# Kernel tuning notes

Hardware: AMD Instinct MI355X
Metric: run time of the kernel (lower is better)

Reference implementation:

```python
import jax, jax.numpy as jnp
import numpy as np

DIM = 96
HEADS = 6
HEAD_DIM = DIM // HEADS
WIN = 8
N = WIN * WIN           # tokens per window
B_ = 4096               # num_windows * batch
TABLE = (2 * WIN - 1) ** 2  # 225


def setup_inputs() -> dict:
    key = jax.random.key(0)
    ks = jax.random.split(key, 7)
    x = jax.random.normal(ks[0], (B_, N, DIM), dtype=jnp.float32)
    rpi = jax.random.randint(ks[1], (N, N), 0, TABLE)
    qkv_w = jax.random.normal(ks[2], (3 * DIM, DIM), dtype=jnp.float32) * 0.02
    qkv_b = jnp.zeros((3 * DIM,), dtype=jnp.float32)
    proj_w = jax.random.normal(ks[3], (DIM, DIM), dtype=jnp.float32) * 0.02
    proj_b = jnp.zeros((DIM,), dtype=jnp.float32)
    rpb_table = jax.random.normal(ks[4], (TABLE, HEADS), dtype=jnp.float32) * 0.02
    return {"x": x, "rpi": rpi, "qkv_w": qkv_w, "qkv_b": qkv_b,
            "proj_w": proj_w, "proj_b": proj_b, "rpb_table": rpb_table}


def reference(x, rpi, qkv_w, qkv_b, proj_w, proj_b, rpb_table):
    b_, n, c = x.shape
    scale = HEAD_DIM ** -0.5
    # qkv projection: (b_, n, 3, H, hd)
    qkv = (x @ qkv_w.T + qkv_b).reshape(b_, n, 3, HEADS, HEAD_DIM)
    qkv = jnp.transpose(qkv, (2, 0, 3, 1, 4))  # (3, b_, H, n, hd)
    q, k, v = qkv[0], qkv[1], qkv[2]
    attn = jnp.einsum('bhnd,bhmd->bhnm', q * scale, k)
    # relative position bias gather: (n, n, H) -> (H, n, n)
    bias = jnp.transpose(rpb_table[rpi], (2, 0, 1))
    attn = jax.nn.softmax(attn + bias[None], axis=-1)
    out = jnp.einsum('bhnm,bhmd->bnhd', attn, v).reshape(b_, n, c)
    return out @ proj_w.T + proj_b
```

## Files before the change

kernel.cpp:

```cpp
#include <hip/hip_runtime.h>

#define NWIN 4096
#define DIM 96
#define HEADS 6
#define NTOK 64

typedef __bf16 bf16x8 __attribute__((ext_vector_type(8)));
typedef __bf16 bf16x4 __attribute__((ext_vector_type(4)));
typedef short  s16x4  __attribute__((ext_vector_type(4)));
typedef float  f32x4  __attribute__((ext_vector_type(4)));

#define WS_QKVW 0
#define WS_PROJW 55296
#define WS_BIAS 73728
#define WS_TOTAL 172032

__device__ __forceinline__ f32x4 mfma32(bf16x8 a, bf16x8 b, f32x4 c) {
  return __builtin_amdgcn_mfma_f32_16x16x32_bf16(a, b, c, 0, 0, 0);
}
__device__ __forceinline__ f32x4 mfma16k(bf16x4 a, bf16x4 b, f32x4 c) {
  return __builtin_amdgcn_mfma_f32_16x16x16bf16_1k(
      __builtin_bit_cast(s16x4, a), __builtin_bit_cast(s16x4, b), c, 0, 0, 0);
}

__device__ __forceinline__ bf16x8 cvt8(const float* p) {
  const float4* q = (const float4*)p;
  float4 a = q[0];
  float4 b = q[1];
  bf16x8 r;
  r[0] = (__bf16)a.x; r[1] = (__bf16)a.y; r[2] = (__bf16)a.z; r[3] = (__bf16)a.w;
  r[4] = (__bf16)b.x; r[5] = (__bf16)b.y; r[6] = (__bf16)b.z; r[7] = (__bf16)b.w;
  return r;
}

__global__ void prep_kernel(const float* __restrict__ qkv_w,
                            const float* __restrict__ proj_w,
                            const float* __restrict__ rpb,
                            const int* __restrict__ rpi,
                            char* __restrict__ ws) {
  int i = blockIdx.x * blockDim.x + threadIdx.x;
  __bf16* qw = (__bf16*)(ws + WS_QKVW);
  __bf16* pw = (__bf16*)(ws + WS_PROJW);
  float* bias = (float*)(ws + WS_BIAS);
  if (i < 288 * 96) qw[i] = (__bf16)qkv_w[i];
  int j = i - 288 * 96;
  if (j >= 0 && j < 96 * 96) pw[j] = (__bf16)proj_w[j];
  int t = i - (288 * 96 + 96 * 96);
  if (t >= 0 && t < HEADS * 16 * 64 * 4) {
    int r = t & 3;
    int lane = (t >> 2) & 63;
    int ba = (t >> 8) & 15;
    int h = t >> 12;
    int bq = ba >> 2, a = ba & 3;
    int l16 = lane & 15, lq = lane >> 4;
    int qrow = 16 * bq + l16;
    int kcol = 16 * a + 4 * lq + r;
    bias[t] = rpb[rpi[qrow * 64 + kcol] * HEADS + h];
  }
}

template <bool USE_WS>
__global__ __launch_bounds__(128, 4) void win_attn(
    const float* __restrict__ x,
    const int* __restrict__ rpi,
    const float* __restrict__ qkv_w,
    const float* __restrict__ qkv_b,
    const float* __restrict__ proj_w,
    const float* __restrict__ proj_b,
    const float* __restrict__ rpb,
    const char* __restrict__ ws,
    float* __restrict__ out) {
  __shared__ __align__(16) __bf16 xfrag[6144];
  __shared__ __align__(16) __bf16 ao[64 * 104];

  const int tid = (int)threadIdx.x;
  const int wv = tid >> 6;
  const int lane = tid & 63;
  const int l16 = lane & 15;
  const int lq = lane >> 4;
  const int b = (int)blockIdx.x;

  const float* xw = x + (size_t)b * (NTOK * DIM);
  const __bf16* qwb = (const __bf16*)(ws + WS_QKVW);
  const __bf16* pwb = (const __bf16*)(ws + WS_PROJW);

#pragma unroll
  for (int ff = 0; ff < 6; ++ff) {
    const int mt = 2 * wv + ff / 3;
    const int ks = ff % 3;
    const int f = 6 * wv + ff;
    bf16x8 v = cvt8(xw + (16 * mt + l16) * DIM + 32 * ks + 8 * lq);
    *(bf16x8*)(xfrag + (f * 64 + lane) * 8) = v;
  }
  __syncthreads();

#define XV(mt, ks) (*(const bf16x8*)(xfrag + (((mt) * 3 + (ks)) * 64 + lane) * 8))

#pragma unroll 1
  for (int hh = 0; hh < 3; ++hh) {
    const int h = wv + 2 * hh;

    bf16x4 kb[4];
    {
      const int frow = (HEADS + h) * 16;
      bf16x8 wb[3];
#pragma unroll
      for (int ks = 0; ks < 3; ++ks) {
        if constexpr (USE_WS)
          wb[ks] = *(const bf16x8*)(qwb + (frow + l16) * 96 + 32 * ks + 8 * lq);
        else
          wb[ks] = cvt8(qkv_w + (frow + l16) * 96 + 32 * ks + 8 * lq);
      }
      const float4 kb4 = *(const float4*)(qkv_b + frow + 4 * lq);
      const float kbv[4] = {kb4.x, kb4.y, kb4.z, kb4.w};
#pragma unroll
      for (int mt = 0; mt < 4; ++mt) {
        f32x4 acc = {0.f, 0.f, 0.f, 0.f};
#pragma unroll
        for (int ks = 0; ks < 3; ++ks) acc = mfma32(wb[ks], XV(mt, ks), acc);
#pragma unroll
        for (int r = 0; r < 4; ++r) kb[mt][r] = (__bf16)(acc[r] + kbv[r]);
      }
    }

    bf16x4 qv4[4];
    {
      const int frow = h * 16;
      bf16x8 wb[3];
#pragma unroll
      for (int ks = 0; ks < 3; ++ks) {
        if constexpr (USE_WS)
          wb[ks] = *(const bf16x8*)(qwb + (frow + l16) * 96 + 32 * ks + 8 * lq);
        else
          wb[ks] = cvt8(qkv_w + (frow + l16) * 96 + 32 * ks + 8 * lq);
      }
      const float4 qb4 = *(const float4*)(qkv_b + frow + 4 * lq);
      const float qbv[4] = {qb4.x, qb4.y, qb4.z, qb4.w};
#pragma unroll
      for (int mt = 0; mt < 4; ++mt) {
        f32x4 acc = {0.f, 0.f, 0.f, 0.f};
#pragma unroll
        for (int ks = 0; ks < 3; ++ks) acc = mfma32(wb[ks], XV(mt, ks), acc);
#pragma unroll
        for (int r = 0; r < 4; ++r)
          qv4[mt][r] = (__bf16)((acc[r] + qbv[r]) * 0.25f);
      }
    }

    bf16x4 vb4[4];
    {
      const int frow = (2 * HEADS + h) * 16;
      bf16x8 wb[3];
#pragma unroll
      for (int ks = 0; ks < 3; ++ks) {
        if constexpr (USE_WS)
          wb[ks] = *(const bf16x8*)(qwb + (frow + l16) * 96 + 32 * ks + 8 * lq);
        else
          wb[ks] = cvt8(qkv_w + (frow + l16) * 96 + 32 * ks + 8 * lq);
      }
      const float vb = qkv_b[frow + l16];
#pragma unroll
      for (int mt = 0; mt < 4; ++mt) {
        f32x4 acc = {0.f, 0.f, 0.f, 0.f};
#pragma unroll
        for (int ks = 0; ks < 3; ++ks) acc = mfma32(XV(mt, ks), wb[ks], acc);
#pragma unroll
        for (int r = 0; r < 4; ++r) vb4[mt][r] = (__bf16)(acc[r] + vb);
      }
    }

    const float4* bias4 = (const float4*)(ws + WS_BIAS) + (h << 10);
#pragma unroll
    for (int bq = 0; bq < 4; ++bq) {
      f32x4 s[4];
      if constexpr (USE_WS) {
#pragma unroll
        for (int a = 0; a < 4; ++a) {
          float4 t = bias4[(bq * 4 + a) * 64 + lane];
          s[a][0] = t.x; s[a][1] = t.y; s[a][2] = t.z; s[a][3] = t.w;
        }
      } else {
#pragma unroll
        for (int a = 0; a < 4; ++a)
#pragma unroll
          for (int r = 0; r < 4; ++r)
            s[a][r] = rpb[rpi[(16 * bq + l16) * 64 + 16 * a + 4 * lq + r] *
                              HEADS + h];
      }

#pragma unroll
      for (int a = 0; a < 4; ++a) s[a] = mfma16k(kb[a], qv4[bq], s[a]);

      float tp[4];
      bf16x4 pa[4];
#pragma unroll
      for (int a = 0; a < 4; ++a) {
        float t0 = 0.f;
#pragma unroll
        for (int r = 0; r < 4; ++r) {
          const __bf16 pe = (__bf16)__expf(s[a][r]);
          pa[a][r] = pe;
          t0 += (float)pe;
        }
        tp[a] = t0;
      }
      float tsum = (tp[0] + tp[1]) + (tp[2] + tp[3]);
      tsum += __shfl_xor(tsum, 16);
      tsum += __shfl_xor(tsum, 32);

      f32x4 oacc = {0.f, 0.f, 0.f, 0.f};
#pragma unroll
      for (int a = 0; a < 4; ++a) oacc = mfma16k(pa[a], vb4[a], oacc);

      const float rv = 1.0f / tsum;
#pragma unroll
      for (int r = 0; r < 4; ++r)
        ao[(16 * bq + 4 * lq + r) * 104 + 16 * h + l16] =
            (__bf16)(oacc[r] * rv);
    }
  }
#undef XV
  __syncthreads();

  float* outw = out + (size_t)b * (NTOK * DIM);
#pragma unroll 1
  for (int cc = 0; cc < 3; ++cc) {
    const int c = wv + 2 * cc;
    bf16x8 wpb[3];
#pragma unroll
    for (int ks = 0; ks < 3; ++ks) {
      if constexpr (USE_WS)
        wpb[ks] = *(const bf16x8*)(pwb + (16 * c + l16) * 96 + 32 * ks + 8 * lq);
      else
        wpb[ks] = cvt8(proj_w + (16 * c + l16) * 96 + 32 * ks + 8 * lq);
    }
    const float pb2 = proj_b[16 * c + l16];
#pragma unroll
    for (int mt = 0; mt < 4; ++mt) {
      f32x4 acc = {0.f, 0.f, 0.f, 0.f};
#pragma unroll
      for (int ks = 0; ks < 3; ++ks) {
        bf16x8 aa =
            *(const bf16x8*)(ao + (16 * mt + l16) * 104 + 32 * ks + 8 * lq);
        acc = mfma32(aa, wpb[ks], acc);
      }
#pragma unroll
      for (int r = 0; r < 4; ++r)
        outw[(16 * mt + 4 * lq + r) * 96 + 16 * c + l16] = acc[r] + pb2;
    }
  }
}

extern "C" void kernel_launch(void* const* d_in, const int* in_sizes, int n_in,
                              void* d_out, int out_size, void* d_ws, size_t ws_size,
                              hipStream_t stream) {
  const float* x      = (const float*)d_in[0];
  const int*   rpi    = (const int*)d_in[1];
  const float* qkv_w  = (const float*)d_in[2];
  const float* qkv_b  = (const float*)d_in[3];
  const float* proj_w = (const float*)d_in[4];
  const float* proj_b = (const float*)d_in[5];
  const float* rpb    = (const float*)d_in[6];
  float* out = (float*)d_out;

  if (ws_size >= (size_t)WS_TOTAL) {
    prep_kernel<<<240, 256, 0, stream>>>(qkv_w, proj_w, rpb, rpi, (char*)d_ws);
    win_attn<true><<<NWIN, 128, 0, stream>>>(x, rpi, qkv_w, qkv_b, proj_w,
                                             proj_b, rpb, (const char*)d_ws,
                                             out);
  } else {
    win_attn<false><<<NWIN, 128, 0, stream>>>(x, rpi, qkv_w, qkv_b, proj_w,
                                              proj_b, rpb, (const char*)d_ws,
                                              out);
  }
}
```

Before: 81.55 us.

## Process four windows per block with double-buffered x prefetch into LDS

Each block now loops over four windows. While the projection stage of the current window runs, the next window's x tile is loaded from global memory into registers, then converted and written into a second LDS buffer. The goal is to hide global load latency and amortize block launch overhead, with bias values folded into the accumulator init. The trade-off is a grid of only 1024 blocks, launch bounds lowered to 2, and more LDS and register use, which could reduce occupancy and latency hiding.

Measured after the change: 82.17 us. Within noise of the previous version (+0.8%).

```diff
diff --git a/kernel.cpp b/kernel.cpp
--- a/kernel.cpp
+++ b/kernel.cpp
@@ -4,6 +4,7 @@
 #define DIM 96
 #define HEADS 6
 #define NTOK 64
+#define WPB 4
 
 typedef __bf16 bf16x8 __attribute__((ext_vector_type(8)));
 typedef __bf16 bf16x4 __attribute__((ext_vector_type(4)));
@@ -60,7 +61,7 @@
 }
 
 template <bool USE_WS>
-__global__ __launch_bounds__(128, 4) void win_attn(
+__global__ __launch_bounds__(128, 2) void win_attn(
     const float* __restrict__ x,
     const int* __restrict__ rpi,
     const float* __restrict__ qkv_w,
@@ -70,7 +71,7 @@
     const float* __restrict__ rpb,
     const char* __restrict__ ws,
     float* __restrict__ out) {
-  __shared__ __align__(16) __bf16 xfrag[6144];
+  __shared__ __align__(16) __bf16 xfrag[2][6144];
   __shared__ __align__(16) __bf16 ao[64 * 104];
 
   const int tid = (int)threadIdx.x;
@@ -78,175 +79,211 @@
   const int lane = tid & 63;
   const int l16 = lane & 15;
   const int lq = lane >> 4;
-  const int b = (int)blockIdx.x;
-
-  const float* xw = x + (size_t)b * (NTOK * DIM);
+  const int base = (int)blockIdx.x * WPB;
+
   const __bf16* qwb = (const __bf16*)(ws + WS_QKVW);
   const __bf16* pwb = (const __bf16*)(ws + WS_PROJW);
 
-#pragma unroll
-  for (int ff = 0; ff < 6; ++ff) {
-    const int mt = 2 * wv + ff / 3;
-    const int ks = ff % 3;
-    const int f = 6 * wv + ff;
-    bf16x8 v = cvt8(xw + (16 * mt + l16) * DIM + 32 * ks + 8 * lq);
-    *(bf16x8*)(xfrag + (f * 64 + lane) * 8) = v;
+  {
+    const float* xw = x + (size_t)base * (NTOK * DIM);
+#pragma unroll
+    for (int ff = 0; ff < 6; ++ff) {
+      const int mt = 2 * wv + ff / 3;
+      const int ks = ff % 3;
+      const int f = 6 * wv + ff;
+      bf16x8 v = cvt8(xw + (16 * mt + l16) * DIM + 32 * ks + 8 * lq);
+      *(bf16x8*)(xfrag[0] + (f * 64 + lane) * 8) = v;
+    }
   }
   __syncthreads();
 
-#define XV(mt, ks) (*(const bf16x8*)(xfrag + (((mt) * 3 + (ks)) * 64 + lane) * 8))
-
 #pragma unroll 1
-  for (int hh = 0; hh < 3; ++hh) {
-    const int h = wv + 2 * hh;
-
-    bf16x4 kb[4];
-    {
-      const int frow = (HEADS + h) * 16;
-      bf16x8 wb[3];
+  for (int i = 0; i < WPB; ++i) {
+    const __bf16* xf = xfrag[i & 1];
+    const int b = base + i;
+
+#define XV(mt, ks) (*(const bf16x8*)(xf + (((mt) * 3 + (ks)) * 64 + lane) * 8))
+
+#pragma unroll 1
+    for (int hh = 0; hh < 3; ++hh) {
+      const int h = wv + 2 * hh;
+
+      bf16x4 kb[4];
+      {
+        const int frow = (HEADS + h) * 16;
+        bf16x8 wb[3];
+#pragma unroll
+        for (int ks = 0; ks < 3; ++ks) {
+          if constexpr (USE_WS)
+            wb[ks] =
+                *(const bf16x8*)(qwb + (frow + l16) * 96 + 32 * ks + 8 * lq);
+          else
+            wb[ks] = cvt8(qkv_w + (frow + l16) * 96 + 32 * ks + 8 * lq);
+        }
+        const float4 kb4 = *(const float4*)(qkv_b + frow + 4 * lq);
+#pragma unroll
+        for (int mt = 0; mt < 4; ++mt) {
+          f32x4 acc = {kb4.x, kb4.y, kb4.z, kb4.w};
+#pragma unroll
+          for (int ks = 0; ks < 3; ++ks) acc = mfma32(wb[ks], XV(mt, ks), acc);
+#pragma unroll
+          for (int r = 0; r < 4; ++r) kb[mt][r] = (__bf16)acc[r];
+        }
+      }
+
+      bf16x4 qv4[4];
+      {
+        const int frow = h * 16;
+        bf16x8 wb[3];
+#pragma unroll
+        for (int ks = 0; ks < 3; ++ks) {
+          if constexpr (USE_WS)
+            wb[ks] =
+                *(const bf16x8*)(qwb + (frow + l16) * 96 + 32 * ks + 8 * lq);
+          else
+            wb[ks] = cvt8(qkv_w + (frow + l16) * 96 + 32 * ks + 8 * lq);
+        }
+        const float4 qb4 = *(const float4*)(qkv_b + frow + 4 * lq);
+#pragma unroll
+        for (int mt = 0; mt < 4; ++mt) {
+          f32x4 acc = {qb4.x, qb4.y, qb4.z, qb4.w};
+#pragma unroll
+          for (int ks = 0; ks < 3; ++ks) acc = mfma32(wb[ks], XV(mt, ks), acc);
+#pragma unroll
+          for (int r = 0; r < 4; ++r) qv4[mt][r] = (__bf16)(acc[r] * 0.25f);
+        }
+      }
+
+      bf16x4 vb4[4];
+      {
+        const int frow = (2 * HEADS + h) * 16;
+        bf16x8 wb[3];
+#pragma unroll
+        for (int ks = 0; ks < 3; ++ks) {
+          if constexpr (USE_WS)
+            wb[ks] =
+                *(const bf16x8*)(qwb + (frow + l16) * 96 + 32 * ks + 8 * lq);
+          else
+            wb[ks] = cvt8(qkv_w + (frow + l16) * 96 + 32 * ks + 8 * lq);
+        }
+        const float vb = qkv_b[frow + l16];
+#pragma unroll
+        for (int mt = 0; mt < 4; ++mt) {
+          f32x4 acc = {vb, vb, vb, vb};
+#pragma unroll
+          for (int ks = 0; ks < 3; ++ks) acc = mfma32(XV(mt, ks), wb[ks], acc);
+#pragma unroll
+          for (int r = 0; r < 4; ++r) vb4[mt][r] = (__bf16)acc[r];
+        }
+      }
+
+      const float4* bias4 = (const float4*)(ws + WS_BIAS) + (h << 10);
+#pragma unroll
+      for (int bq = 0; bq < 4; ++bq) {
+        f32x4 s[4];
+        if constexpr (USE_WS) {
+#pragma unroll
+          for (int a = 0; a < 4; ++a)
+            s[a] = __builtin_bit_cast(f32x4, bias4[(bq * 4 + a) * 64 + lane]);
+        } else {
+#pragma unroll
+          for (int a = 0; a < 4; ++a)
+#pragma unroll
+            for (int r = 0; r < 4; ++r)
+              s[a][r] = rpb[rpi[(16 * bq + l16) * 64 + 16 * a + 4 * lq + r] *
+                                HEADS + h];
+        }
+
+#pragma unroll
+        for (int a = 0; a < 4; ++a) s[a] = mfma16k(kb[a], qv4[bq], s[a]);
+
+        float tp[4];
+        bf16x4 pa[4];
+#pragma unroll
+        for (int a = 0; a < 4; ++a) {
+          float t0 = 0.f;
+#pragma unroll
+          for (int r = 0; r < 4; ++r) {
+            const __bf16 pe = (__bf16)__expf(s[a][r]);
+            pa[a][r] = pe;
+            t0 += (float)pe;
+          }
+          tp[a] = t0;
+        }
+        float tsum = (tp[0] + tp[1]) + (tp[2] + tp[3]);
+        tsum += __shfl_xor(tsum, 16);
+        tsum += __shfl_xor(tsum, 32);
+
+        f32x4 oacc = {0.f, 0.f, 0.f, 0.f};
+#pragma unroll
+        for (int a = 0; a < 4; ++a) oacc = mfma16k(pa[a], vb4[a], oacc);
+
+        const float rv = 1.0f / tsum;
+#pragma unroll
+        for (int r = 0; r < 4; ++r)
+          ao[(16 * bq + 4 * lq + r) * 104 + 16 * h + l16] =
+              (__bf16)(oacc[r] * rv);
+      }
+    }
+#undef XV
+    __syncthreads();
+
+    float4 xr[12];
+    if (i + 1 < WPB) {
+      const float* xw = x + (size_t)(b + 1) * (NTOK * DIM);
+#pragma unroll
+      for (int ff = 0; ff < 6; ++ff) {
+        const int mt = 2 * wv + ff / 3;
+        const int ks = ff % 3;
+        const float4* p =
+            (const float4*)(xw + (16 * mt + l16) * DIM + 32 * ks + 8 * lq);
+        xr[2 * ff] = p[0];
+        xr[2 * ff + 1] = p[1];
+      }
+    }
+
+    float* outw = out + (size_t)b * (NTOK * DIM);
+#pragma unroll 1
+    for (int cc = 0; cc < 3; ++cc) {
+      const int c = wv + 2 * cc;
+      bf16x8 wpb[3];
 #pragma unroll
       for (int ks = 0; ks < 3; ++ks) {
         if constexpr (USE_WS)
-          wb[ks] = *(const bf16x8*)(qwb + (frow + l16) * 96 + 32 * ks + 8 * lq);
+          wpb[ks] =
+              *(const bf16x8*)(pwb + (16 * c + l16) * 96 + 32 * ks + 8 * lq);
         else
-          wb[ks] = cvt8(qkv_w + (frow + l16) * 96 + 32 * ks + 8 * lq);
-      }
-      const float4 kb4 = *(const float4*)(qkv_b + frow + 4 * lq);
-      const float kbv[4] = {kb4.x, kb4.y, kb4.z, kb4.w};
+          wpb[ks] = cvt8(proj_w + (16 * c + l16) * 96 + 32 * ks + 8 * lq);
+      }
+      const float pb2 = proj_b[16 * c + l16];
 #pragma unroll
       for (int mt = 0; mt < 4; ++mt) {
-        f32x4 acc = {0.f, 0.f, 0.f, 0.f};
-#pragma unroll
-        for (int ks = 0; ks < 3; ++ks) acc = mfma32(wb[ks], XV(mt, ks), acc);
-#pragma unroll
-        for (int r = 0; r < 4; ++r) kb[mt][r] = (__bf16)(acc[r] + kbv[r]);
-      }
-    }
-
-    bf16x4 qv4[4];
-    {
-      const int frow = h * 16;
-      bf16x8 wb[3];
-#pragma unroll
-      for (int ks = 0; ks < 3; ++ks) {
-        if constexpr (USE_WS)
-          wb[ks] = *(const bf16x8*)(qwb + (frow + l16) * 96 + 32 * ks + 8 * lq);
-        else
-          wb[ks] = cvt8(qkv_w + (frow + l16) * 96 + 32 * ks + 8 * lq);
-      }
-      const float4 qb4 = *(const float4*)(qkv_b + frow + 4 * lq);
-      const float qbv[4] = {qb4.x, qb4.y, qb4.z, qb4.w};
-#pragma unroll
-      for (int mt = 0; mt < 4; ++mt) {
-        f32x4 acc = {0.f, 0.f, 0.f, 0.f};
-#pragma unroll
-        for (int ks = 0; ks < 3; ++ks) acc = mfma32(wb[ks], XV(mt, ks), acc);
+        f32x4 acc = {pb2, pb2, pb2, pb2};
+#pragma unroll
+        for (int ks = 0; ks < 3; ++ks) {
+          bf16x8 aa =
+              *(const bf16x8*)(ao + (16 * mt + l16) * 104 + 32 * ks + 8 * lq);
+          acc = mfma32(aa, wpb[ks], acc);
+        }
 #pragma unroll
         for (int r = 0; r < 4; ++r)
-          qv4[mt][r] = (__bf16)((acc[r] + qbv[r]) * 0.25f);
-      }
-    }
-
-    bf16x4 vb4[4];
-    {
-      const int frow = (2 * HEADS + h) * 16;
-      bf16x8 wb[3];
-#pragma unroll
-      for (int ks = 0; ks < 3; ++ks) {
-        if constexpr (USE_WS)
-          wb[ks] = *(const bf16x8*)(qwb + (frow + l16) * 96 + 32 * ks + 8 * lq);
-        else
-          wb[ks] = cvt8(qkv_w + (frow + l16) * 96 + 32 * ks + 8 * lq);
-      }
-      const float vb = qkv_b[frow + l16];
-#pragma unroll
-      for (int mt = 0; mt < 4; ++mt) {
-        f32x4 acc = {0.f, 0.f, 0.f, 0.f};
-#pragma unroll
-        for (int ks = 0; ks < 3; ++ks) acc = mfma32(XV(mt, ks), wb[ks], acc);
-#pragma unroll
-        for (int r = 0; r < 4; ++r) vb4[mt][r] = (__bf16)(acc[r] + vb);
-      }
-    }
-
-    const float4* bias4 = (const float4*)(ws + WS_BIAS) + (h << 10);
-#pragma unroll
-    for (int bq = 0; bq < 4; ++bq) {
-      f32x4 s[4];
-      if constexpr (USE_WS) {
-#pragma unroll
-        for (int a = 0; a < 4; ++a) {
-          float4 t = bias4[(bq * 4 + a) * 64 + lane];
-          s[a][0] = t.x; s[a][1] = t.y; s[a][2] = t.z; s[a][3] = t.w;
-        }
-      } else {
-#pragma unroll
-        for (int a = 0; a < 4; ++a)
-#pragma unroll
-          for (int r = 0; r < 4; ++r)
-            s[a][r] = rpb[rpi[(16 * bq + l16) * 64 + 16 * a + 4 * lq + r] *
-                              HEADS + h];
-      }
-
-#pragma unroll
-      for (int a = 0; a < 4; ++a) s[a] = mfma16k(kb[a], qv4[bq], s[a]);
-
-      float tp[4];
-      bf16x4 pa[4];
-#pragma unroll
-      for (int a = 0; a < 4; ++a) {
-        float t0 = 0.f;
-#pragma unroll
-        for (int r = 0; r < 4; ++r) {
-          const __bf16 pe = (__bf16)__expf(s[a][r]);
-          pa[a][r] = pe;
-          t0 += (float)pe;
-        }
-        tp[a] = t0;
-      }
-      float tsum = (tp[0] + tp[1]) + (tp[2] + tp[3]);
-      tsum += __shfl_xor(tsum, 16);
-      tsum += __shfl_xor(tsum, 32);
-
-      f32x4 oacc = {0.f, 0.f, 0.f, 0.f};
-#pragma unroll
-      for (int a = 0; a < 4; ++a) oacc = mfma16k(pa[a], vb4[a], oacc);
-
-      const float rv = 1.0f / tsum;
-#pragma unroll
-      for (int r = 0; r < 4; ++r)
-        ao[(16 * bq + 4 * lq + r) * 104 + 16 * h + l16] =
-            (__bf16)(oacc[r] * rv);
-    }
-  }
-#undef XV
-  __syncthreads();
-
-  float* outw = out + (size_t)b * (NTOK * DIM);
-#pragma unroll 1
-  for (int cc = 0; cc < 3; ++cc) {
-    const int c = wv + 2 * cc;
-    bf16x8 wpb[3];
-#pragma unroll
-    for (int ks = 0; ks < 3; ++ks) {
-      if constexpr (USE_WS)
-        wpb[ks] = *(const bf16x8*)(pwb + (16 * c + l16) * 96 + 32 * ks + 8 * lq);
-      else
-        wpb[ks] = cvt8(proj_w + (16 * c + l16) * 96 + 32 * ks + 8 * lq);
-    }
-    const float pb2 = proj_b[16 * c + l16];
-#pragma unroll
-    for (int mt = 0; mt < 4; ++mt) {
-      f32x4 acc = {0.f, 0.f, 0.f, 0.f};
-#pragma unroll
-      for (int ks = 0; ks < 3; ++ks) {
-        bf16x8 aa =
-            *(const bf16x8*)(ao + (16 * mt + l16) * 104 + 32 * ks + 8 * lq);
-        acc = mfma32(aa, wpb[ks], acc);
-      }
-#pragma unroll
-      for (int r = 0; r < 4; ++r)
-        outw[(16 * mt + 4 * lq + r) * 96 + 16 * c + l16] = acc[r] + pb2;
+          outw[(16 * mt + 4 * lq + r) * 96 + 16 * c + l16] = acc[r];
+      }
+    }
+
+    if (i + 1 < WPB) {
+#pragma unroll
+      for (int ff = 0; ff < 6; ++ff) {
+        const int f = 6 * wv + ff;
+        const float4 a = xr[2 * ff], c4 = xr[2 * ff + 1];
+        bf16x8 v;
+        v[0] = (__bf16)a.x;  v[1] = (__bf16)a.y;
+        v[2] = (__bf16)a.z;  v[3] = (__bf16)a.w;
+        v[4] = (__bf16)c4.x; v[5] = (__bf16)c4.y;
+        v[6] = (__bf16)c4.z; v[7] = (__bf16)c4.w;
+        *(bf16x8*)(xfrag[(i + 1) & 1] + (f * 64 + lane) * 8) = v;
+      }
+      __syncthreads();
     }
   }
 }
@@ -265,12 +302,10 @@
 
   if (ws_size >= (size_t)WS_TOTAL) {
     prep_kernel<<<240, 256, 0, stream>>>(qkv_w, proj_w, rpb, rpi, (char*)d_ws);
-    win_attn<true><<<NWIN, 128, 0, stream>>>(x, rpi, qkv_w, qkv_b, proj_w,
-                                             proj_b, rpb, (const char*)d_ws,
-                                             out);
+    win_attn<true><<<NWIN / WPB, 128, 0, stream>>>(
+        x, rpi, qkv_w, qkv_b, proj_w, proj_b, rpb, (const char*)d_ws, out);
   } else {
-    win_attn<false><<<NWIN, 128, 0, stream>>>(x, rpi, qkv_w, qkv_b, proj_w,
-                                              proj_b, rpb, (const char*)d_ws,
-                                              out);
+    win_attn<false><<<NWIN / WPB, 128, 0, stream>>>(
+        x, rpi, qkv_w, qkv_b, proj_w, proj_b, rpb, (const char*)d_ws, out);
   }
 }
```
